# Kernel optimization log

Measured on AMD Instinct MI355X. Metric: run time of the kernel, lower is better.

Reference implementation:

```python
import jax, jax.numpy as jnp
import numpy as np

B, OBS, ACT_DIM, C, CTX, H = 128, 512, 7, 100, 128, 512
IN = OBS + 1 + CTX  # states + scalar action component + context = 641


def cont2disc(values, n):
    return jnp.clip(jnp.floor((values + 1.0) / 2.0 * n), 0, n - 1)


def setup_inputs() -> dict:
    key = jax.random.key(0)
    ks = jax.random.split(key, 10)
    def w(k, shape):
        return jax.random.normal(k, shape, dtype=jnp.float32) / np.sqrt(shape[-2])
    return {
        "observations": jax.random.normal(ks[0], (B, OBS), dtype=jnp.float32),
        "actions": jax.random.uniform(ks[1], (B, ACT_DIM), dtype=jnp.float32, minval=-1.0, maxval=1.0),
        # one MLP per action dim (weight_sharing=False): layers IN->H->H->CTX
        "W1": w(ks[2], (ACT_DIM, IN, H)),  "b1": jnp.zeros((ACT_DIM, H), jnp.float32),
        "W2": w(ks[3], (ACT_DIM, H, H)),   "b2": jnp.zeros((ACT_DIM, H), jnp.float32),
        "W3": w(ks[4], (ACT_DIM, H, CTX)), "b3": jnp.zeros((ACT_DIM, CTX), jnp.float32),
        # output_proj = MLP((1,)): single dense CTX->1, no activation
        "Wp": w(ks[5], (CTX, 1)), "bp": jnp.zeros((1,), jnp.float32),
        "compute_lse": 1,
    }


def reference(observations, actions, W1, b1, W2, b2, W3, b3, Wp, bp, compute_lse):
    n = observations.shape[0]
    acts = cont2disc(actions, C)  # [B, ACT_DIM], float component indices
    context = jnp.zeros((n, CTX), observations.dtype)
    comp = jnp.arange(C, dtype=observations.dtype)  # candidate components 0..C-1
    q = jnp.zeros((n, ACT_DIM * C), observations.dtype)

    for i in range(1, ACT_DIM):
        def mlp(x, i=i):  # hidden layers relu, final layer linear
            h = jax.nn.relu(x @ W1[i] + b1[i])
            h = jax.nn.relu(h @ W2[i] + b2[i])
            return h @ W3[i] + b3[i]

        # batched over all num_components candidate actions (replaces the per-j loop)
        xin = jnp.concatenate([
            jnp.broadcast_to(observations[:, None, :], (n, C, OBS)),
            jnp.broadcast_to(comp[None, :, None], (n, C, 1)),
            jnp.broadcast_to(context[:, None, :], (n, C, CTX)),
        ], axis=-1)  # [B, C, IN]
        curr_ctx = mlp(xin) + context[:, None, :]        # [B, C, CTX]
        qv = (curr_ctx @ Wp + bp)[..., 0]                # [B, C]
        q = q.at[:, (i - 1) * C : i * C].set(qv)          # which_qval ordering

        # advance context with the actual (discretized) action
        x = jnp.concatenate([observations, acts[:, i:i + 1], context], axis=-1)
        context = mlp(x) + context

    if compute_lse:
        return jax.scipy.special.logsumexp(q, axis=-1)    # [B]
    return context @ Wp + bp                              # [B, 1]
```

## Files before the change

kernel.cpp:

```cpp
#include <hip/hip_runtime.h>
#include <math.h>

#define BATCH 128
#define ACT 7
#define NC 100
#define CTXD 128
#define HID 512
#define QW 600

typedef __attribute__((ext_vector_type(8))) __bf16 bf16x8;
typedef __attribute__((ext_vector_type(4))) float f32x4;
typedef __attribute__((ext_vector_type(8))) unsigned short u16x8;
typedef __attribute__((ext_vector_type(4))) unsigned short u16x4;

__device__ __forceinline__ unsigned short f2bf(float f) {
    union { float f; unsigned int u; } v; v.f = f;
    unsigned int u = v.u;
    return (unsigned short)((u + 0x7fffu + ((u >> 16) & 1u)) >> 16);
}

__device__ __forceinline__ unsigned short f2bf_fast(float f) {
    return (unsigned short)((__float_as_uint(f) + 0x8000u) >> 16);
}
__device__ __forceinline__ unsigned int pack2bf(float a, float b) {
    unsigned int ua = __float_as_uint(a) + 0x8000u;
    unsigned int ub = __float_as_uint(b) + 0x8000u;
    return (ua >> 16) | (ub & 0xffff0000u);
}

__device__ __forceinline__ void async16(const void* g, void* l) {
    __builtin_amdgcn_global_load_lds(
        (const __attribute__((address_space(1))) unsigned int*)(uintptr_t)g,
        (__attribute__((address_space(3))) unsigned int*)(unsigned int)(uintptr_t)l,
        16, 0, 0);
}

__global__ void cvt_kernel(const float* __restrict__ obs, const float* __restrict__ W1,
                           const float* __restrict__ W2, const float* __restrict__ W3,
                           unsigned short* __restrict__ obs_bf, unsigned short* __restrict__ W1Cbf,
                           unsigned short* __restrict__ W2bf, unsigned short* __restrict__ W3bf) {
    const int e = (blockIdx.x * 256 + threadIdx.x) * 4;
    const float* src; unsigned short* dst;
    if (e < 65536)        { src = obs + e; dst = obs_bf + e; }
    else if (e < 458752)  { int f = e - 65536; int i = f >> 16; int rem = f & 65535;
                            src = W1 + (size_t)(i + 1) * 328192 + 513*512 + rem; dst = W1Cbf + f; }
    else if (e < 2031616) { int f = e - 458752; src = W2 + 262144 + f; dst = W2bf + f; }
    else                  { int f = e - 2031616; src = W3 + 65536 + f; dst = W3bf + f; }
    float4 v = *(const float4*)src;
    u16x4 o; o[0] = f2bf(v.x); o[1] = f2bf(v.y); o[2] = f2bf(v.z); o[3] = f2bf(v.w);
    *(u16x4*)dst = o;
}

__global__ void prep_transpose(const float* __restrict__ W1, const float* __restrict__ W2,
                               const float* __restrict__ W3,
                               unsigned short* __restrict__ W1AT, unsigned short* __restrict__ W2T,
                               unsigned short* __restrict__ W3T) {
    __shared__ float tile[32][33];
    const int z = blockIdx.z;
    const float* ip; unsigned short* op; int Cn;
    if (z < 6)       { ip = W1 + (size_t)(z + 1) * 328192; op = W1AT + (size_t)z * 262144; Cn = 512; }
    else if (z < 12) { int i = z - 6;  ip = W2 + (size_t)(i + 1) * 262144; op = W2T + (size_t)i * 262144; Cn = 512; }
    else             { int i = z - 12; ip = W3 + (size_t)(i + 1) * 65536;  op = W3T + (size_t)i * 65536;  Cn = 128;
                       if (blockIdx.y >= 4) return; }
    const int r0 = blockIdx.x * 32, c0 = blockIdx.y * 32;
    const int tx = threadIdx.x, ty = threadIdx.y;
    #pragma unroll
    for (int j = 0; j < 32; j += 8)
        tile[ty + j][tx] = ip[(size_t)(r0 + ty + j) * Cn + c0 + tx];
    __syncthreads();
    #pragma unroll
    for (int j = 0; j < 32; j += 8)
        op[(size_t)(c0 + ty + j) * 512 + r0 + tx] = f2bf(tile[tx][ty + j]);
}

__launch_bounds__(256)
__global__ void yobs_kernel(const unsigned short* __restrict__ A,
                            const unsigned short* __restrict__ BtAll,
                            const float* __restrict__ b1,
                            float* __restrict__ Yobs) {
    __shared__ unsigned short As[64*32];
    __shared__ unsigned short Bs[128*32];
    const int m0 = blockIdx.x * 64;
    const int n0 = blockIdx.y * 128;
    const int z  = blockIdx.z;
    const unsigned short* Bt = BtAll + (size_t)z * 262144;
    const int tid = threadIdx.x, lane = tid & 63, wave = tid >> 6;
    const int wm = wave >> 1, wn = wave & 1;
    const int srow = tid >> 2, skc = (tid & 3) * 8;
    const unsigned short* gA  = A  + (size_t)(m0 + srow) * HID + skc;
    const unsigned short* gB0 = Bt + (size_t)(n0 + srow) * HID + skc;
    const unsigned short* gB1 = gB0 + 64 * HID;
    f32x4 acc[2][4] = {};
    for (int k0 = 0; k0 < HID; k0 += 32) {
        async16(gA + k0, As + tid*8);
        async16(gB0 + k0, Bs + tid*8);
        async16(gB1 + k0, Bs + 2048 + tid*8);
        __syncthreads();
        const int q8 = (lane >> 4) * 8, l15 = lane & 15;
        bf16x8 af[2], bfr[4];
        #pragma unroll
        for (int mt = 0; mt < 2; ++mt)
            af[mt] = *(const bf16x8*)(As + (wm*32 + mt*16 + l15) * 32 + q8);
        #pragma unroll
        for (int nt = 0; nt < 4; ++nt)
            bfr[nt] = *(const bf16x8*)(Bs + (wn*64 + nt*16 + l15) * 32 + q8);
        #pragma unroll
        for (int mt = 0; mt < 2; ++mt)
            #pragma unroll
            for (int nt = 0; nt < 4; ++nt)
                acc[mt][nt] = __builtin_amdgcn_mfma_f32_16x16x32_bf16(af[mt], bfr[nt], acc[mt][nt], 0, 0, 0);
        __syncthreads();
    }
    const int colL = wn*64 + (lane & 15);
    #pragma unroll
    for (int nt = 0; nt < 4; ++nt) {
        const int col = n0 + colL + nt*16;
        const float bb = b1[(z + 1) * HID + col];
        #pragma unroll
        for (int mt = 0; mt < 2; ++mt)
            #pragma unroll
            for (int r = 0; r < 4; ++r) {
                const int row = m0 + wm*32 + mt*16 + (lane >> 4)*4 + r;
                Yobs[(size_t)z * 65536 + (size_t)row * HID + col] = acc[mt][nt][r] + bb;
            }
    }
}

__launch_bounds__(1024)
__global__ void chain_kernel(const float* __restrict__ Yobs, const float* __restrict__ W1,
                             const unsigned short* __restrict__ W1Cbf,
                             const unsigned short* __restrict__ W2bf,
                             const unsigned short* __restrict__ W3bf,
                             const float* __restrict__ b2, const float* __restrict__ b3,
                             const float* __restrict__ actions,
                             float* __restrict__ Y0all, float* __restrict__ CTXS) {
    const int b = blockIdx.x, t = threadIdx.x;
    __shared__ float ctx[128], h1[512], h2s[512];
    __shared__ float part[2048];
    const int pair = t & 255, kq = t >> 8;
    const int pair3 = t & 63, kq3 = t >> 6;
    if (t < 128) ctx[t] = 0.f;
    __syncthreads();
    for (int i = 1; i <= 6; ++i) {
        if (t < 128) CTXS[(size_t)(i-1)*16384 + b*128 + t] = ctx[t];
        const float a = actions[b*ACT + i];
        float fj = floorf((a + 1.0f) * 50.0f);
        fj = fminf(fmaxf(fj, 0.0f), 99.0f);
        {
            const unsigned int* wp1 = (const unsigned int*)(W1Cbf + (size_t)(i-1)*65536) + pair;
            float acc0 = 0.f, acc1 = 0.f;
            #pragma unroll 8
            for (int k = kq*32; k < kq*32 + 32; ++k) {
                unsigned int u = wp1[k*256];
                float c = ctx[k];
                acc0 = fmaf(c, __uint_as_float(u << 16), acc0);
                acc1 = fmaf(c, __uint_as_float(u & 0xffff0000u), acc1);
            }
            *(float2*)(&part[kq*512 + 2*pair]) = make_float2(acc0, acc1);
        }
        __syncthreads();
        if (t < 256) {
            const int n2 = 2*t;
            float2 p0 = *(const float2*)(&part[n2]);
            float2 p1 = *(const float2*)(&part[512 + n2]);
            float2 p2 = *(const float2*)(&part[1024 + n2]);
            float2 p3 = *(const float2*)(&part[1536 + n2]);
            float2 yo = *(const float2*)(Yobs + (size_t)(i-1)*65536 + b*512 + n2);
            float y0a = yo.x + p0.x + p1.x + p2.x + p3.x;
            float y0b = yo.y + p0.y + p1.y + p2.y + p3.y;
            *(float2*)(Y0all + (size_t)(i-1)*65536 + b*512 + n2) = make_float2(y0a, y0b);
            const float* w1a = W1 + (size_t)i*328192 + 262144;
            float2 wv = *(const float2*)(w1a + n2);
            h1[n2]   = fmaxf(fmaf(fj, wv.x, y0a), 0.f);
            h1[n2+1] = fmaxf(fmaf(fj, wv.y, y0b), 0.f);
        }
        __syncthreads();
        {
            const unsigned int* wp2 = (const unsigned int*)(W2bf + (size_t)(i-1)*262144) + pair;
            float acc0 = 0.f, acc1 = 0.f;
            #pragma unroll 16
            for (int k = kq*128; k < kq*128 + 128; ++k) {
                unsigned int u = wp2[k*256];
                float hv = h1[k];
                acc0 = fmaf(hv, __uint_as_float(u << 16), acc0);
                acc1 = fmaf(hv, __uint_as_float(u & 0xffff0000u), acc1);
            }
            *(float2*)(&part[kq*512 + 2*pair]) = make_float2(acc0, acc1);
        }
        __syncthreads();
        if (t < 256) {
            const int n2 = 2*t;
            float2 p0 = *(const float2*)(&part[n2]);
            float2 p1 = *(const float2*)(&part[512 + n2]);
            float2 p2 = *(const float2*)(&part[1024 + n2]);
            float2 p3 = *(const float2*)(&part[1536 + n2]);
            float2 bb = *(const float2*)(b2 + i*512 + n2);
            h2s[n2]   = fmaxf(p0.x + p1.x + p2.x + p3.x + bb.x, 0.f);
            h2s[n2+1] = fmaxf(p0.y + p1.y + p2.y + p3.y + bb.y, 0.f);
        }
        __syncthreads();
        {
            const unsigned int* wp3 = (const unsigned int*)(W3bf + (size_t)(i-1)*65536) + pair3;
            float acc0 = 0.f, acc1 = 0.f;
            #pragma unroll 8
            for (int k = kq3*32; k < kq3*32 + 32; ++k) {
                unsigned int u = wp3[k*64];
                float hv = h2s[k];
                acc0 = fmaf(hv, __uint_as_float(u << 16), acc0);
                acc1 = fmaf(hv, __uint_as_float(u & 0xffff0000u), acc1);
            }
            *(float2*)(&part[kq3*128 + 2*pair3]) = make_float2(acc0, acc1);
        }
        __syncthreads();
        if (t < 128) {
            float s = 0.f;
            #pragma unroll
            for (int qg = 0; qg < 16; ++qg) s += part[qg*128 + t];
            ctx[t] = s + b3[i*128 + t] + ctx[t];
        }
        __syncthreads();
    }
}

__launch_bounds__(256, 2)
__global__ void h2all_kernel(const float* __restrict__ Y0all, const float* __restrict__ W1,
                             const unsigned short* __restrict__ W2T, const float* __restrict__ b2,
                             unsigned short* __restrict__ H2) {
    __shared__ unsigned short ASl[128*32];
    __shared__ unsigned short BSl[256*32];
    const int bx = blockIdx.x;
    const int z  = bx / 100;
    const int r2 = (bx % 100) * 128;
    const int r0 = z * 12800 + r2;
    const int n0 = blockIdx.y * 256;
    const int tid = threadIdx.x, lane = tid & 63, wave = tid >> 6;
    const int wm = wave >> 1, wn = wave & 1;
    const int l15 = lane & 15, q8 = (lane >> 4) * 8;
    const int rA = tid >> 2, kc8 = (tid & 3) * 8;
    const int g1 = r2 + rA, g2 = r2 + rA + 64;
    const float c1 = (float)(g1 % 100), c2 = (float)(g2 % 100);
    const float* y1p = Y0all + (size_t)z*65536 + (size_t)(g1/100)*512 + kc8;
    const float* y2p = Y0all + (size_t)z*65536 + (size_t)(g2/100)*512 + kc8;
    const float* w1a = W1 + (size_t)(z+1)*328192 + 262144 + kc8;
    const unsigned short* Bbase = W2T + (size_t)z*262144 + (size_t)n0*512;
    f32x4 acc[4][8] = {};
    for (int k0 = 0; k0 < 512; k0 += 32) {
        {
            float4 wa = *(const float4*)(w1a + k0);
            float4 wb = *(const float4*)(w1a + k0 + 4);
            float4 ya = *(const float4*)(y1p + k0);
            float4 yb = *(const float4*)(y1p + k0 + 4);
            uint4 o;
            o.x = pack2bf(fmaxf(fmaf(c1, wa.x, ya.x), 0.f), fmaxf(fmaf(c1, wa.y, ya.y), 0.f));
            o.y = pack2bf(fmaxf(fmaf(c1, wa.z, ya.z), 0.f), fmaxf(fmaf(c1, wa.w, ya.w), 0.f));
            o.z = pack2bf(fmaxf(fmaf(c1, wb.x, yb.x), 0.f), fmaxf(fmaf(c1, wb.y, yb.y), 0.f));
            o.w = pack2bf(fmaxf(fmaf(c1, wb.z, yb.z), 0.f), fmaxf(fmaf(c1, wb.w, yb.w), 0.f));
            *(uint4*)(ASl + rA*32 + kc8) = o;
            float4 yc = *(const float4*)(y2p + k0);
            float4 yd = *(const float4*)(y2p + k0 + 4);
            o.x = pack2bf(fmaxf(fmaf(c2, wa.x, yc.x), 0.f), fmaxf(fmaf(c2, wa.y, yc.y), 0.f));
            o.y = pack2bf(fmaxf(fmaf(c2, wa.z, yc.z), 0.f), fmaxf(fmaf(c2, wa.w, yc.w), 0.f));
            o.z = pack2bf(fmaxf(fmaf(c2, wb.x, yd.x), 0.f), fmaxf(fmaf(c2, wb.y, yd.y), 0.f));
            o.w = pack2bf(fmaxf(fmaf(c2, wb.z, yd.z), 0.f), fmaxf(fmaf(c2, wb.w, yd.w), 0.f));
            *(uint4*)(ASl + (rA + 64)*32 + kc8) = o;
        }
        #pragma unroll
        for (int c = 0; c < 4; ++c) {
            const int s = c*256 + tid;
            const int col = s >> 2, sub = s & 3;
            async16(Bbase + (size_t)col*512 + k0 + sub*8, BSl + (size_t)s*8);
        }
        __syncthreads();
        bf16x8 af[4], bfr[8];
        #pragma unroll
        for (int mt = 0; mt < 4; ++mt)
            af[mt] = *(const bf16x8*)(ASl + (wm*64 + mt*16 + l15)*32 + q8);
        #pragma unroll
        for (int nt = 0; nt < 8; ++nt)
            bfr[nt] = *(const bf16x8*)(BSl + (wn*128 + nt*16 + l15)*32 + q8);
        #pragma unroll
        for (int mt = 0; mt < 4; ++mt)
            #pragma unroll
            for (int nt = 0; nt < 8; ++nt)
                acc[mt][nt] = __builtin_amdgcn_mfma_f32_16x16x32_bf16(af[mt], bfr[nt], acc[mt][nt], 0, 0, 0);
        __syncthreads();
    }
    #pragma unroll
    for (int nt = 0; nt < 8; ++nt) {
        const int col = n0 + wn*128 + nt*16 + l15;
        const float bb = b2[(z+1)*512 + col];
        #pragma unroll
        for (int mt = 0; mt < 4; ++mt)
            #pragma unroll
            for (int r = 0; r < 4; ++r) {
                const int row = r0 + wm*64 + mt*16 + (lane >> 4)*4 + r;
                H2[(size_t)row * 512 + col] = f2bf_fast(fmaxf(acc[mt][nt][r] + bb, 0.f));
            }
    }
}

__launch_bounds__(256)
__global__ void gemm3all_kernel(const unsigned short* __restrict__ H2,
                                const unsigned short* __restrict__ W3T,
                                const float* __restrict__ b3, const float* __restrict__ CTXS,
                                const float* __restrict__ Wp, const float* __restrict__ bp,
                                float* __restrict__ q) {
    __shared__ unsigned short ASl[64*32];
    __shared__ unsigned short BSl[128*32];
    __shared__ float CCs[64][132];
    __shared__ float qp[64][4];
    const int bx = blockIdx.x;
    const int z  = bx / 200;
    const int r0 = bx * 64;
    const int r2 = (bx % 200) * 64;
    const int tid = threadIdx.x, lane = tid & 63, wave = tid >> 6;
    const int wm = wave >> 1, wn = wave & 1;
    const int l15 = lane & 15, q8 = (lane >> 4) * 8;
    const unsigned short* W3Tz = W3T + (size_t)z*65536;
    f32x4 acc[2][4] = {};
    for (int k0 = 0; k0 < 512; k0 += 32) {
        {
            const int s = wave*64 + lane, row = s >> 2, sub = s & 3;
            async16(H2 + (size_t)(r0 + row)*512 + k0 + sub*8, ASl + (size_t)s*8);
        }
        #pragma unroll
        for (int c = 0; c < 2; ++c) {
            const int s = c*256 + wave*64 + lane, col = s >> 2, sub = s & 3;
            async16(W3Tz + (size_t)col*512 + k0 + sub*8, BSl + (size_t)s*8);
        }
        __syncthreads();
        bf16x8 af[2], bfr[4];
        #pragma unroll
        for (int mt = 0; mt < 2; ++mt)
            af[mt] = *(const bf16x8*)(ASl + (wm*32 + mt*16 + l15)*32 + q8);
        #pragma unroll
        for (int nt = 0; nt < 4; ++nt)
            bfr[nt] = *(const bf16x8*)(BSl + (wn*64 + nt*16 + l15)*32 + q8);
        #pragma unroll
        for (int mt = 0; mt < 2; ++mt)
            #pragma unroll
            for (int nt = 0; nt < 4; ++nt)
                acc[mt][nt] = __builtin_amdgcn_mfma_f32_16x16x32_bf16(af[mt], bfr[nt], acc[mt][nt], 0, 0, 0);
        __syncthreads();
    }
    #pragma unroll
    for (int nt = 0; nt < 4; ++nt) {
        const int col = wn*64 + nt*16 + l15;
        const float bb = b3[(z+1)*128 + col];
        #pragma unroll
        for (int mt = 0; mt < 2; ++mt)
            #pragma unroll
            for (int r = 0; r < 4; ++r) {
                const int rowL = wm*32 + mt*16 + (lane >> 4)*4 + r;
                const int gb = (r2 + rowL) / 100;
                CCs[rowL][col] = acc[mt][nt][r] + bb + CTXS[(size_t)z*16384 + gb*128 + col];
            }
    }
    __syncthreads();
    {
        const int rowL = tid >> 2, seg = tid & 3;
        float s = 0.f;
        #pragma unroll
        for (int j = 0; j < 32; ++j) s += CCs[rowL][seg*32 + j] * Wp[seg*32 + j];
        qp[rowL][seg] = s;
    }
    __syncthreads();
    if (tid < 64) {
        const int gr2 = r2 + tid;
        const int gb = gr2 / 100, gc = gr2 - gb * 100;
        float s = qp[tid][0] + qp[tid][1] + qp[tid][2] + qp[tid][3];
        q[gb * QW + z * 100 + gc] = s + bp[0];
    }
}

__global__ void lse_kernel(const float* __restrict__ q, float* __restrict__ out) {
    __shared__ float red[256];
    int b = blockIdx.x, t = threadIdx.x;
    float m = 0.0f;
    for (int k = t; k < QW; k += 256) m = fmaxf(m, q[b*QW + k]);
    red[t] = m; __syncthreads();
    for (int s = 128; s > 0; s >>= 1) { if (t < s) red[t] = fmaxf(red[t], red[t+s]); __syncthreads(); }
    m = red[0]; __syncthreads();
    float sum = 0.0f;
    for (int k = t; k < QW; k += 256) sum += expf(q[b*QW + k] - m);
    red[t] = sum; __syncthreads();
    for (int s = 128; s > 0; s >>= 1) { if (t < s) red[t] += red[t+s]; __syncthreads(); }
    if (t == 0) out[b] = logf(red[0] + 100.0f * expf(-m)) + m;
}

extern "C" void kernel_launch(void* const* d_in, const int* in_sizes, int n_in,
                              void* d_out, int out_size, void* d_ws, size_t ws_size,
                              hipStream_t stream) {
    const float* obs     = (const float*)d_in[0];
    const float* actions = (const float*)d_in[1];
    const float* W1      = (const float*)d_in[2];
    const float* b1      = (const float*)d_in[3];
    const float* W2      = (const float*)d_in[4];
    const float* b2      = (const float*)d_in[5];
    const float* W3      = (const float*)d_in[6];
    const float* b3      = (const float*)d_in[7];
    const float* Wp      = (const float*)d_in[8];
    const float* bp      = (const float*)d_in[9];
    float* out = (float*)d_out;
    float* ws  = (float*)d_ws;

    unsigned short* obs_bf = (unsigned short*)(ws);
    unsigned short* W1AT   = (unsigned short*)(ws + 32768);
    unsigned short* W2T    = (unsigned short*)(ws + 819200);
    unsigned short* W3T    = (unsigned short*)(ws + 1605632);
    unsigned short* W1Cbf  = (unsigned short*)(ws + 1802240);
    unsigned short* W2bf   = (unsigned short*)(ws + 1998848);
    unsigned short* W3bf   = (unsigned short*)(ws + 2785280);
    float* Yobs  = ws + 2981888;
    float* Y0all = ws + 3375104;
    float* CTXS  = ws + 3768320;
    float* q     = ws + 3866624;
    unsigned short* H2 = (unsigned short*)(ws + 3943424);

    cvt_kernel<<<2368, 256, 0, stream>>>(obs, W1, W2, W3, obs_bf, W1Cbf, W2bf, W3bf);
    prep_transpose<<<dim3(16,16,18), dim3(32,8), 0, stream>>>(W1, W2, W3, W1AT, W2T, W3T);
    yobs_kernel<<<dim3(2,4,6), 256, 0, stream>>>(obs_bf, W1AT, b1, Yobs);
    chain_kernel<<<BATCH, 1024, 0, stream>>>(Yobs, W1, W1Cbf, W2bf, W3bf, b2, b3, actions, Y0all, CTXS);
    h2all_kernel<<<dim3(600, 2), 256, 0, stream>>>(Y0all, W1, W2T, b2, H2);
    gemm3all_kernel<<<1200, 256, 0, stream>>>(H2, W3T, b3, CTXS, Wp, bp, q);
    lse_kernel<<<BATCH, 256, 0, stream>>>(q, out);
}
```

Baseline: 259.4 us.

## Double-buffer LDS tiles in h2all and gemm3all to overlap loads with MFMA

```diff
diff --git a/kernel.cpp b/kernel.cpp
--- a/kernel.cpp
+++ b/kernel.cpp
@@ -226,8 +226,8 @@
 __global__ void h2all_kernel(const float* __restrict__ Y0all, const float* __restrict__ W1,
                              const unsigned short* __restrict__ W2T, const float* __restrict__ b2,
                              unsigned short* __restrict__ H2) {
-    __shared__ unsigned short ASl[128*32];
-    __shared__ unsigned short BSl[256*32];
+    __shared__ unsigned short ASl[2][128*32];
+    __shared__ unsigned short BSl[2][256*32];
     const int bx = blockIdx.x;
     const int z  = bx / 100;
     const int r2 = (bx % 100) * 128;
@@ -243,46 +243,57 @@
     const float* y2p = Y0all + (size_t)z*65536 + (size_t)(g2/100)*512 + kc8;
     const float* w1a = W1 + (size_t)(z+1)*328192 + 262144 + kc8;
     const unsigned short* Bbase = W2T + (size_t)z*262144 + (size_t)n0*512;
-    f32x4 acc[4][8] = {};
-    for (int k0 = 0; k0 < 512; k0 += 32) {
-        {
-            float4 wa = *(const float4*)(w1a + k0);
-            float4 wb = *(const float4*)(w1a + k0 + 4);
-            float4 ya = *(const float4*)(y1p + k0);
-            float4 yb = *(const float4*)(y1p + k0 + 4);
-            uint4 o;
-            o.x = pack2bf(fmaxf(fmaf(c1, wa.x, ya.x), 0.f), fmaxf(fmaf(c1, wa.y, ya.y), 0.f));
-            o.y = pack2bf(fmaxf(fmaf(c1, wa.z, ya.z), 0.f), fmaxf(fmaf(c1, wa.w, ya.w), 0.f));
-            o.z = pack2bf(fmaxf(fmaf(c1, wb.x, yb.x), 0.f), fmaxf(fmaf(c1, wb.y, yb.y), 0.f));
-            o.w = pack2bf(fmaxf(fmaf(c1, wb.z, yb.z), 0.f), fmaxf(fmaf(c1, wb.w, yb.w), 0.f));
-            *(uint4*)(ASl + rA*32 + kc8) = o;
-            float4 yc = *(const float4*)(y2p + k0);
-            float4 yd = *(const float4*)(y2p + k0 + 4);
-            o.x = pack2bf(fmaxf(fmaf(c2, wa.x, yc.x), 0.f), fmaxf(fmaf(c2, wa.y, yc.y), 0.f));
-            o.y = pack2bf(fmaxf(fmaf(c2, wa.z, yc.z), 0.f), fmaxf(fmaf(c2, wa.w, yc.w), 0.f));
-            o.z = pack2bf(fmaxf(fmaf(c2, wb.x, yd.x), 0.f), fmaxf(fmaf(c2, wb.y, yd.y), 0.f));
-            o.w = pack2bf(fmaxf(fmaf(c2, wb.z, yd.z), 0.f), fmaxf(fmaf(c2, wb.w, yd.w), 0.f));
-            *(uint4*)(ASl + (rA + 64)*32 + kc8) = o;
-        }
+
+    float4 wa, wb, ya, yb, yc, yd;
+    auto loadA = [&](int k0) {
+        wa = *(const float4*)(w1a + k0); wb = *(const float4*)(w1a + k0 + 4);
+        ya = *(const float4*)(y1p + k0); yb = *(const float4*)(y1p + k0 + 4);
+        yc = *(const float4*)(y2p + k0); yd = *(const float4*)(y2p + k0 + 4);
+    };
+    auto packA = [&](int buf) {
+        uint4 o;
+        o.x = pack2bf(fmaxf(fmaf(c1, wa.x, ya.x), 0.f), fmaxf(fmaf(c1, wa.y, ya.y), 0.f));
+        o.y = pack2bf(fmaxf(fmaf(c1, wa.z, ya.z), 0.f), fmaxf(fmaf(c1, wa.w, ya.w), 0.f));
+        o.z = pack2bf(fmaxf(fmaf(c1, wb.x, yb.x), 0.f), fmaxf(fmaf(c1, wb.y, yb.y), 0.f));
+        o.w = pack2bf(fmaxf(fmaf(c1, wb.z, yb.z), 0.f), fmaxf(fmaf(c1, wb.w, yb.w), 0.f));
+        *(uint4*)(&ASl[buf][rA*32 + kc8]) = o;
+        o.x = pack2bf(fmaxf(fmaf(c2, wa.x, yc.x), 0.f), fmaxf(fmaf(c2, wa.y, yc.y), 0.f));
+        o.y = pack2bf(fmaxf(fmaf(c2, wa.z, yc.z), 0.f), fmaxf(fmaf(c2, wa.w, yc.w), 0.f));
+        o.z = pack2bf(fmaxf(fmaf(c2, wb.x, yd.x), 0.f), fmaxf(fmaf(c2, wb.y, yd.y), 0.f));
+        o.w = pack2bf(fmaxf(fmaf(c2, wb.z, yd.z), 0.f), fmaxf(fmaf(c2, wb.w, yd.w), 0.f));
+        *(uint4*)(&ASl[buf][(rA + 64)*32 + kc8]) = o;
+    };
+    auto stageB = [&](int buf, int k0) {
         #pragma unroll
         for (int c = 0; c < 4; ++c) {
             const int s = c*256 + tid;
             const int col = s >> 2, sub = s & 3;
-            async16(Bbase + (size_t)col*512 + k0 + sub*8, BSl + (size_t)s*8);
-        }
-        __syncthreads();
+            async16(Bbase + (size_t)col*512 + k0 + sub*8, &BSl[buf][s*8]);
+        }
+    };
+
+    f32x4 acc[4][8] = {};
+    stageB(0, 0);
+    loadA(0);
+    packA(0);
+    __syncthreads();
+    #pragma unroll 2
+    for (int s = 0; s < 16; ++s) {
+        const int cur = s & 1, nxt = cur ^ 1;
+        if (s < 15) { stageB(nxt, (s+1)*32); loadA((s+1)*32); }
         bf16x8 af[4], bfr[8];
         #pragma unroll
         for (int mt = 0; mt < 4; ++mt)
-            af[mt] = *(const bf16x8*)(ASl + (wm*64 + mt*16 + l15)*32 + q8);
+            af[mt] = *(const bf16x8*)(&ASl[cur][(wm*64 + mt*16 + l15)*32 + q8]);
         #pragma unroll
         for (int nt = 0; nt < 8; ++nt)
-            bfr[nt] = *(const bf16x8*)(BSl + (wn*128 + nt*16 + l15)*32 + q8);
+            bfr[nt] = *(const bf16x8*)(&BSl[cur][(wn*128 + nt*16 + l15)*32 + q8]);
         #pragma unroll
         for (int mt = 0; mt < 4; ++mt)
             #pragma unroll
             for (int nt = 0; nt < 8; ++nt)
                 acc[mt][nt] = __builtin_amdgcn_mfma_f32_16x16x32_bf16(af[mt], bfr[nt], acc[mt][nt], 0, 0, 0);
+        if (s < 15) packA(nxt);
         __syncthreads();
     }
     #pragma unroll
@@ -305,8 +316,8 @@
                                 const float* __restrict__ b3, const float* __restrict__ CTXS,
                                 const float* __restrict__ Wp, const float* __restrict__ bp,
                                 float* __restrict__ q) {
-    __shared__ unsigned short ASl[64*32];
-    __shared__ unsigned short BSl[128*32];
+    __shared__ unsigned short ASl[2][64*32];
+    __shared__ unsigned short BSl[2][128*32];
     __shared__ float CCs[64][132];
     __shared__ float qp[64][4];
     const int bx = blockIdx.x;
@@ -317,25 +328,33 @@
     const int wm = wave >> 1, wn = wave & 1;
     const int l15 = lane & 15, q8 = (lane >> 4) * 8;
     const unsigned short* W3Tz = W3T + (size_t)z*65536;
-    f32x4 acc[2][4] = {};
-    for (int k0 = 0; k0 < 512; k0 += 32) {
+
+    auto stage = [&](int buf, int k0) {
         {
             const int s = wave*64 + lane, row = s >> 2, sub = s & 3;
-            async16(H2 + (size_t)(r0 + row)*512 + k0 + sub*8, ASl + (size_t)s*8);
+            async16(H2 + (size_t)(r0 + row)*512 + k0 + sub*8, &ASl[buf][s*8]);
         }
         #pragma unroll
         for (int c = 0; c < 2; ++c) {
             const int s = c*256 + wave*64 + lane, col = s >> 2, sub = s & 3;
-            async16(W3Tz + (size_t)col*512 + k0 + sub*8, BSl + (size_t)s*8);
-        }
-        __syncthreads();
+            async16(W3Tz + (size_t)col*512 + k0 + sub*8, &BSl[buf][s*8]);
+        }
+    };
+
+    f32x4 acc[2][4] = {};
+    stage(0, 0);
+    __syncthreads();
+    #pragma unroll 2
+    for (int s = 0; s < 16; ++s) {
+        const int cur = s & 1, nxt = cur ^ 1;
+        if (s < 15) stage(nxt, (s+1)*32);
         bf16x8 af[2], bfr[4];
         #pragma unroll
         for (int mt = 0; mt < 2; ++mt)
-            af[mt] = *(const bf16x8*)(ASl + (wm*32 + mt*16 + l15)*32 + q8);
+            af[mt] = *(const bf16x8*)(&ASl[cur][(wm*32 + mt*16 + l15)*32 + q8]);
         #pragma unroll
         for (int nt = 0; nt < 4; ++nt)
-            bfr[nt] = *(const bf16x8*)(BSl + (wn*64 + nt*16 + l15)*32 + q8);
+            bfr[nt] = *(const bf16x8*)(&BSl[cur][(wn*64 + nt*16 + l15)*32 + q8]);
         #pragma unroll
         for (int mt = 0; mt < 2; ++mt)
             #pragma unroll
```

Result: no change. 257.1 us (-0.9%).

## Materialize H1, use LDS-free register-pipelined GEMMs, fold context projection into scalar offset

Applied to the files above, without the earlier changes.

```diff
diff --git a/kernel.cpp b/kernel.cpp
--- a/kernel.cpp
+++ b/kernel.cpp
@@ -18,7 +18,6 @@
     unsigned int u = v.u;
     return (unsigned short)((u + 0x7fffu + ((u >> 16) & 1u)) >> 16);
 }
-
 __device__ __forceinline__ unsigned short f2bf_fast(float f) {
     return (unsigned short)((__float_as_uint(f) + 0x8000u) >> 16);
 }
@@ -133,7 +132,8 @@
                              const unsigned short* __restrict__ W3bf,
                              const float* __restrict__ b2, const float* __restrict__ b3,
                              const float* __restrict__ actions,
-                             float* __restrict__ Y0all, float* __restrict__ CTXS) {
+                             const float* __restrict__ Wp, const float* __restrict__ bp,
+                             float* __restrict__ Y0all, float* __restrict__ QOFF) {
     const int b = blockIdx.x, t = threadIdx.x;
     __shared__ float ctx[128], h1[512], h2s[512];
     __shared__ float part[2048];
@@ -142,7 +142,15 @@
     if (t < 128) ctx[t] = 0.f;
     __syncthreads();
     for (int i = 1; i <= 6; ++i) {
-        if (t < 128) CTXS[(size_t)(i-1)*16384 + b*128 + t] = ctx[t];
+        if (t < 128) part[t] = (ctx[t] + b3[i*128 + t]) * Wp[t];
+        __syncthreads();
+        if (t < 64) {
+            float v = part[t] + part[t + 64];
+            #pragma unroll
+            for (int o = 32; o > 0; o >>= 1) v += __shfl_down(v, o, 64);
+            if (t == 0) QOFF[(i-1)*128 + b] = v + bp[0];
+        }
+        __syncthreads();
         const float a = actions[b*ACT + i];
         float fj = floorf((a + 1.0f) * 50.0f);
         fj = fminf(fmaxf(fj, 0.0f), 99.0f);
@@ -222,155 +230,148 @@
     }
 }
 
-__launch_bounds__(256, 2)
-__global__ void h2all_kernel(const float* __restrict__ Y0all, const float* __restrict__ W1,
-                             const unsigned short* __restrict__ W2T, const float* __restrict__ b2,
+__global__ void h1all_kernel(const float* __restrict__ Y0all, const float* __restrict__ W1,
+                             unsigned short* __restrict__ H1) {
+    const int t = blockIdx.x * 256 + threadIdx.x;
+    const int row = t >> 6, kc = (t & 63) << 3;
+    const int z = row / 12800, rr = row - z * 12800;
+    const int b = rr / 100;
+    const float c = (float)(rr - b * 100);
+    const float* yp = Y0all + (size_t)z*65536 + (size_t)b*512 + kc;
+    const float* wp = W1 + (size_t)(z+1)*328192 + 262144 + kc;
+    float4 ya = *(const float4*)(yp), yb = *(const float4*)(yp + 4);
+    float4 wa = *(const float4*)(wp), wb = *(const float4*)(wp + 4);
+    uint4 o;
+    o.x = pack2bf(fmaxf(fmaf(c, wa.x, ya.x), 0.f), fmaxf(fmaf(c, wa.y, ya.y), 0.f));
+    o.y = pack2bf(fmaxf(fmaf(c, wa.z, ya.z), 0.f), fmaxf(fmaf(c, wa.w, ya.w), 0.f));
+    o.z = pack2bf(fmaxf(fmaf(c, wb.x, yb.x), 0.f), fmaxf(fmaf(c, wb.y, yb.y), 0.f));
+    o.w = pack2bf(fmaxf(fmaf(c, wb.z, yb.z), 0.f), fmaxf(fmaf(c, wb.w, yb.w), 0.f));
+    *(uint4*)(H1 + (size_t)row * 512 + kc) = o;
+}
+
+__launch_bounds__(256)
+__global__ void gemm2_kernel(const unsigned short* __restrict__ H1,
+                             const unsigned short* __restrict__ W2T,
+                             const float* __restrict__ b2,
                              unsigned short* __restrict__ H2) {
-    __shared__ unsigned short ASl[128*32];
-    __shared__ unsigned short BSl[256*32];
-    const int bx = blockIdx.x;
-    const int z  = bx / 100;
-    const int r2 = (bx % 100) * 128;
-    const int r0 = z * 12800 + r2;
-    const int n0 = blockIdx.y * 256;
     const int tid = threadIdx.x, lane = tid & 63, wave = tid >> 6;
-    const int wm = wave >> 1, wn = wave & 1;
+    const int wt = blockIdx.x * 4 + wave;
+    const int r0 = wt * 64;
+    const int z  = r0 / 12800;
+    const int n0 = blockIdx.y * 128;
     const int l15 = lane & 15, q8 = (lane >> 4) * 8;
-    const int rA = tid >> 2, kc8 = (tid & 3) * 8;
-    const int g1 = r2 + rA, g2 = r2 + rA + 64;
-    const float c1 = (float)(g1 % 100), c2 = (float)(g2 % 100);
-    const float* y1p = Y0all + (size_t)z*65536 + (size_t)(g1/100)*512 + kc8;
-    const float* y2p = Y0all + (size_t)z*65536 + (size_t)(g2/100)*512 + kc8;
-    const float* w1a = W1 + (size_t)(z+1)*328192 + 262144 + kc8;
-    const unsigned short* Bbase = W2T + (size_t)z*262144 + (size_t)n0*512;
+    const unsigned short* Ap[4];
+    const unsigned short* Bp[8];
+    #pragma unroll
+    for (int mt = 0; mt < 4; ++mt)
+        Ap[mt] = H1 + (size_t)(r0 + mt*16 + l15)*512 + q8;
+    #pragma unroll
+    for (int nt = 0; nt < 8; ++nt)
+        Bp[nt] = W2T + (size_t)z*262144 + (size_t)(n0 + nt*16 + l15)*512 + q8;
     f32x4 acc[4][8] = {};
-    for (int k0 = 0; k0 < 512; k0 += 32) {
-        {
-            float4 wa = *(const float4*)(w1a + k0);
-            float4 wb = *(const float4*)(w1a + k0 + 4);
-            float4 ya = *(const float4*)(y1p + k0);
-            float4 yb = *(const float4*)(y1p + k0 + 4);
-            uint4 o;
-            o.x = pack2bf(fmaxf(fmaf(c1, wa.x, ya.x), 0.f), fmaxf(fmaf(c1, wa.y, ya.y), 0.f));
-            o.y = pack2bf(fmaxf(fmaf(c1, wa.z, ya.z), 0.f), fmaxf(fmaf(c1, wa.w, ya.w), 0.f));
-            o.z = pack2bf(fmaxf(fmaf(c1, wb.x, yb.x), 0.f), fmaxf(fmaf(c1, wb.y, yb.y), 0.f));
-            o.w = pack2bf(fmaxf(fmaf(c1, wb.z, yb.z), 0.f), fmaxf(fmaf(c1, wb.w, yb.w), 0.f));
-            *(uint4*)(ASl + rA*32 + kc8) = o;
-            float4 yc = *(const float4*)(y2p + k0);
-            float4 yd = *(const float4*)(y2p + k0 + 4);
-            o.x = pack2bf(fmaxf(fmaf(c2, wa.x, yc.x), 0.f), fmaxf(fmaf(c2, wa.y, yc.y), 0.f));
-            o.y = pack2bf(fmaxf(fmaf(c2, wa.z, yc.z), 0.f), fmaxf(fmaf(c2, wa.w, yc.w), 0.f));
-            o.z = pack2bf(fmaxf(fmaf(c2, wb.x, yd.x), 0.f), fmaxf(fmaf(c2, wb.y, yd.y), 0.f));
-            o.w = pack2bf(fmaxf(fmaf(c2, wb.z, yd.z), 0.f), fmaxf(fmaf(c2, wb.w, yd.w), 0.f));
-            *(uint4*)(ASl + (rA + 64)*32 + kc8) = o;
-        }
-        #pragma unroll
-        for (int c = 0; c < 4; ++c) {
-            const int s = c*256 + tid;
-            const int col = s >> 2, sub = s & 3;
-            async16(Bbase + (size_t)col*512 + k0 + sub*8, BSl + (size_t)s*8);
-        }
-        __syncthreads();
-        bf16x8 af[4], bfr[8];
-        #pragma unroll
-        for (int mt = 0; mt < 4; ++mt)
-            af[mt] = *(const bf16x8*)(ASl + (wm*64 + mt*16 + l15)*32 + q8);
-        #pragma unroll
-        for (int nt = 0; nt < 8; ++nt)
-            bfr[nt] = *(const bf16x8*)(BSl + (wn*128 + nt*16 + l15)*32 + q8);
+    bf16x8 af[4], bfr[8], af2[4], bfr2[8];
+    #pragma unroll
+    for (int mt = 0; mt < 4; ++mt) af[mt] = *(const bf16x8*)(Ap[mt]);
+    #pragma unroll
+    for (int nt = 0; nt < 8; ++nt) bfr[nt] = *(const bf16x8*)(Bp[nt]);
+    #pragma unroll 2
+    for (int s = 0; s < 16; ++s) {
+        if (s < 15) {
+            const int k1 = (s + 1) * 32;
+            #pragma unroll
+            for (int mt = 0; mt < 4; ++mt) af2[mt] = *(const bf16x8*)(Ap[mt] + k1);
+            #pragma unroll
+            for (int nt = 0; nt < 8; ++nt) bfr2[nt] = *(const bf16x8*)(Bp[nt] + k1);
+        }
         #pragma unroll
         for (int mt = 0; mt < 4; ++mt)
             #pragma unroll
             for (int nt = 0; nt < 8; ++nt)
                 acc[mt][nt] = __builtin_amdgcn_mfma_f32_16x16x32_bf16(af[mt], bfr[nt], acc[mt][nt], 0, 0, 0);
-        __syncthreads();
+        #pragma unroll
+        for (int mt = 0; mt < 4; ++mt) af[mt] = af2[mt];
+        #pragma unroll
+        for (int nt = 0; nt < 8; ++nt) bfr[nt] = bfr2[nt];
     }
     #pragma unroll
     for (int nt = 0; nt < 8; ++nt) {
-        const int col = n0 + wn*128 + nt*16 + l15;
+        const int col = n0 + nt*16 + l15;
         const float bb = b2[(z+1)*512 + col];
         #pragma unroll
         for (int mt = 0; mt < 4; ++mt)
             #pragma unroll
             for (int r = 0; r < 4; ++r) {
-                const int row = r0 + wm*64 + mt*16 + (lane >> 4)*4 + r;
+                const int row = r0 + mt*16 + (lane >> 4)*4 + r;
                 H2[(size_t)row * 512 + col] = f2bf_fast(fmaxf(acc[mt][nt][r] + bb, 0.f));
             }
     }
 }
 
 __launch_bounds__(256)
-__global__ void gemm3all_kernel(const unsigned short* __restrict__ H2,
-                                const unsigned short* __restrict__ W3T,
-                                const float* __restrict__ b3, const float* __restrict__ CTXS,
-                                const float* __restrict__ Wp, const float* __restrict__ bp,
-                                float* __restrict__ q) {
-    __shared__ unsigned short ASl[64*32];
-    __shared__ unsigned short BSl[128*32];
-    __shared__ float CCs[64][132];
-    __shared__ float qp[64][4];
-    const int bx = blockIdx.x;
-    const int z  = bx / 200;
-    const int r0 = bx * 64;
-    const int r2 = (bx % 200) * 64;
+__global__ void gemm3_kernel(const unsigned short* __restrict__ H2,
+                             const unsigned short* __restrict__ W3T,
+                             const float* __restrict__ Wp,
+                             const float* __restrict__ QOFF,
+                             float* __restrict__ q) {
     const int tid = threadIdx.x, lane = tid & 63, wave = tid >> 6;
-    const int wm = wave >> 1, wn = wave & 1;
+    const int wt = blockIdx.x * 4 + wave;
+    const int r0 = wt * 64;
+    const int z  = r0 / 12800;
+    const int r2 = r0 - z * 12800;
     const int l15 = lane & 15, q8 = (lane >> 4) * 8;
-    const unsigned short* W3Tz = W3T + (size_t)z*65536;
-    f32x4 acc[2][4] = {};
-    for (int k0 = 0; k0 < 512; k0 += 32) {
-        {
-            const int s = wave*64 + lane, row = s >> 2, sub = s & 3;
-            async16(H2 + (size_t)(r0 + row)*512 + k0 + sub*8, ASl + (size_t)s*8);
-        }
-        #pragma unroll
-        for (int c = 0; c < 2; ++c) {
-            const int s = c*256 + wave*64 + lane, col = s >> 2, sub = s & 3;
-            async16(W3Tz + (size_t)col*512 + k0 + sub*8, BSl + (size_t)s*8);
-        }
-        __syncthreads();
-        bf16x8 af[2], bfr[4];
-        #pragma unroll
-        for (int mt = 0; mt < 2; ++mt)
-            af[mt] = *(const bf16x8*)(ASl + (wm*32 + mt*16 + l15)*32 + q8);
-        #pragma unroll
-        for (int nt = 0; nt < 4; ++nt)
-            bfr[nt] = *(const bf16x8*)(BSl + (wn*64 + nt*16 + l15)*32 + q8);
-        #pragma unroll
-        for (int mt = 0; mt < 2; ++mt)
-            #pragma unroll
-            for (int nt = 0; nt < 4; ++nt)
+    const unsigned short* Ap[4];
+    const unsigned short* Bp[8];
+    #pragma unroll
+    for (int mt = 0; mt < 4; ++mt)
+        Ap[mt] = H2 + (size_t)(r0 + mt*16 + l15)*512 + q8;
+    #pragma unroll
+    for (int nt = 0; nt < 8; ++nt)
+        Bp[nt] = W3T + (size_t)z*65536 + (size_t)(nt*16 + l15)*512 + q8;
+    f32x4 acc[4][8] = {};
+    bf16x8 af[4], bfr[8], af2[4], bfr2[8];
+    #pragma unroll
+    for (int mt = 0; mt < 4; ++mt) af[mt] = *(const bf16x8*)(Ap[mt]);
+    #pragma unroll
+    for (int nt = 0; nt < 8; ++nt) bfr[nt] = *(const bf16x8*)(Bp[nt]);
+    #pragma unroll 2
+    for (int s = 0; s < 16; ++s) {
+        if (s < 15) {
+            const int k1 = (s + 1) * 32;
+            #pragma unroll
+            for (int mt = 0; mt < 4; ++mt) af2[mt] = *(const bf16x8*)(Ap[mt] + k1);
+            #pragma unroll
+            for (int nt = 0; nt < 8; ++nt) bfr2[nt] = *(const bf16x8*)(Bp[nt] + k1);
+        }
+        #pragma unroll
+        for (int mt = 0; mt < 4; ++mt)
+            #pragma unroll
+            for (int nt = 0; nt < 8; ++nt)
                 acc[mt][nt] = __builtin_amdgcn_mfma_f32_16x16x32_bf16(af[mt], bfr[nt], acc[mt][nt], 0, 0, 0);
-        __syncthreads();
-    }
-    #pragma unroll
-    for (int nt = 0; nt < 4; ++nt) {
-        const int col = wn*64 + nt*16 + l15;
-        const float bb = b3[(z+1)*128 + col];
-        #pragma unroll
-        for (int mt = 0; mt < 2; ++mt)
-            #pragma unroll
-            for (int r = 0; r < 4; ++r) {
-                const int rowL = wm*32 + mt*16 + (lane >> 4)*4 + r;
-                const int gb = (r2 + rowL) / 100;
-                CCs[rowL][col] = acc[mt][nt][r] + bb + CTXS[(size_t)z*16384 + gb*128 + col];
-            }
-    }
-    __syncthreads();
-    {
-        const int rowL = tid >> 2, seg = tid & 3;
-        float s = 0.f;
-        #pragma unroll
-        for (int j = 0; j < 32; ++j) s += CCs[rowL][seg*32 + j] * Wp[seg*32 + j];
-        qp[rowL][seg] = s;
-    }
-    __syncthreads();
-    if (tid < 64) {
-        const int gr2 = r2 + tid;
-        const int gb = gr2 / 100, gc = gr2 - gb * 100;
-        float s = qp[tid][0] + qp[tid][1] + qp[tid][2] + qp[tid][3];
-        q[gb * QW + z * 100 + gc] = s + bp[0];
-    }
+        #pragma unroll
+        for (int mt = 0; mt < 4; ++mt) af[mt] = af2[mt];
+        #pragma unroll
+        for (int nt = 0; nt < 8; ++nt) bfr[nt] = bfr2[nt];
+    }
+    float wpv[8];
+    #pragma unroll
+    for (int nt = 0; nt < 8; ++nt) wpv[nt] = Wp[nt*16 + l15];
+    #pragma unroll
+    for (int mt = 0; mt < 4; ++mt)
+        #pragma unroll
+        for (int r = 0; r < 4; ++r) {
+            float p = 0.f;
+            #pragma unroll
+            for (int nt = 0; nt < 8; ++nt) p = fmaf(acc[mt][nt][r], wpv[nt], p);
+            p += __shfl_xor(p, 1, 64);
+            p += __shfl_xor(p, 2, 64);
+            p += __shfl_xor(p, 4, 64);
+            p += __shfl_xor(p, 8, 64);
+            if (l15 == 0) {
+                const int row2 = r2 + mt*16 + (lane >> 4)*4 + r;
+                const int gb = row2 / 100, gc = row2 - gb * 100;
+                q[gb * QW + z * 100 + gc] = p + QOFF[z*128 + gb];
+            }
+        }
 }
 
 __global__ void lse_kernel(const float* __restrict__ q, float* __restrict__ out) {
@@ -413,15 +414,17 @@
     unsigned short* W3bf   = (unsigned short*)(ws + 2785280);
     float* Yobs  = ws + 2981888;
     float* Y0all = ws + 3375104;
-    float* CTXS  = ws + 3768320;
-    float* q     = ws + 3866624;
-    unsigned short* H2 = (unsigned short*)(ws + 3943424);
+    float* QOFF  = ws + 3768320;
+    float* q     = ws + 3769344;
+    unsigned short* H1 = (unsigned short*)(ws + 3846144);
+    unsigned short* H2 = (unsigned short*)(ws + 23506944);
 
     cvt_kernel<<<2368, 256, 0, stream>>>(obs, W1, W2, W3, obs_bf, W1Cbf, W2bf, W3bf);
     prep_transpose<<<dim3(16,16,18), dim3(32,8), 0, stream>>>(W1, W2, W3, W1AT, W2T, W3T);
     yobs_kernel<<<dim3(2,4,6), 256, 0, stream>>>(obs_bf, W1AT, b1, Yobs);
-    chain_kernel<<<BATCH, 1024, 0, stream>>>(Yobs, W1, W1Cbf, W2bf, W3bf, b2, b3, actions, Y0all, CTXS);
-    h2all_kernel<<<dim3(600, 2), 256, 0, stream>>>(Y0all, W1, W2T, b2, H2);
-    gemm3all_kernel<<<1200, 256, 0, stream>>>(H2, W3T, b3, CTXS, Wp, bp, q);
+    chain_kernel<<<BATCH, 1024, 0, stream>>>(Yobs, W1, W1Cbf, W2bf, W3bf, b2, b3, actions, Wp, bp, Y0all, QOFF);
+    h1all_kernel<<<19200, 256, 0, stream>>>(Y0all, W1, H1);
+    gemm2_kernel<<<dim3(300, 4), 256, 0, stream>>>(H1, W2T, b2, H2);
+    gemm3_kernel<<<300, 256, 0, stream>>>(H2, W3T, Wp, QOFF, q);
     lse_kernel<<<BATCH, 256, 0, stream>>>(q, out);
 }
```

After: 359.5 us. +38.6%, slower.
